# Kernel optimization log

Hardware: AMD Instinct MI355X
Metric: run time of the kernel (lower is better)

## Reference

```python
import jax, jax.numpy as jnp
import numpy as np

D = 2048          # n_embd
F = 1408          # moe_inter_dim
E = 8             # n_routed_experts
TOPK = 2          # n_activated_experts
N_SHARED = 2
ROUTE_SCALE = 1.0


def setup_inputs() -> dict:
    key = jax.random.key(0)
    ks = jax.random.split(key, 8)
    s = 0.02
    x = jax.random.normal(ks[0], (2, 1024, D), dtype=jnp.float32)
    gate_w = jax.random.normal(ks[1], (D, E), dtype=jnp.float32) * s
    Fs = F * N_SHARED
    sw1 = jax.random.normal(ks[2], (D, Fs), dtype=jnp.float32) * s
    sw2 = jax.random.normal(ks[3], (Fs, D), dtype=jnp.float32) * s
    sw3 = jax.random.normal(ks[4], (D, Fs), dtype=jnp.float32) * s
    rw1 = jax.random.normal(ks[5], (E, D, F), dtype=jnp.float32) * s
    rw2 = jax.random.normal(ks[6], (E, F, D), dtype=jnp.float32) * s
    rw3 = jax.random.normal(ks[7], (E, D, F), dtype=jnp.float32) * s
    return {"x": x, "gate_w": gate_w, "sw1": sw1, "sw2": sw2, "sw3": sw3,
            "rw1": rw1, "rw2": rw2, "rw3": rw3}


def _swiglu(x, w1, w2, w3):
    return (jax.nn.silu(x @ w1) * (x @ w3)) @ w2


def reference(x, gate_w, sw1, sw2, sw3, rw1, rw2, rw3):
    B, T, _ = x.shape
    xf = x.reshape(-1, D)                       # [N, D]
    N = xf.shape[0]
    # shared experts (always applied)
    y = _swiglu(xf, sw1, sw2, sw3)              # [N, D]
    # gate: softmax scores, top-k (bias is None since n_embd != 7168; n_groups == 1)
    scores = jax.nn.softmax(xf @ gate_w, axis=-1)       # [N, E]
    weights, indices = jax.lax.top_k(scores, TOPK)       # gathered original scores
    weights = weights * ROUTE_SCALE
    # combine weights per (token, expert); zero for unassigned -> same math as
    # the per-expert gather/scatter loop in the original module
    cw = jnp.zeros((N, E), dtype=xf.dtype).at[jnp.arange(N)[:, None], indices].add(weights)
    for e in range(E):  # fixed small structural loop over experts
        h = _swiglu(xf, rw1[e], rw2[e], rw3[e])  # [N, D]
        y = y + cw[:, e:e + 1] * h
    return y.reshape(B, T, D)
```

## Files before the change

kernel.cpp:

```cpp
#include <hip/hip_runtime.h>
#include <hip/hip_bf16.h>
#include <math.h>

#define D_DIM 2048
#define F_DIM 1408
#define FS_DIM 2816
#define E_NUM 8
#define N_TOK 2048

typedef __attribute__((ext_vector_type(8))) short bf16x8;
typedef __attribute__((ext_vector_type(4))) float f32x4;

#define WAITVM(n) asm volatile("s_waitcnt vmcnt(" #n ")" ::: "memory")

__device__ inline short f2bf(float f) {
    __hip_bfloat16 h = __float2bfloat16(f);
    return *reinterpret_cast<short*>(&h);
}
__device__ inline float bf2f(short s) {
    __hip_bfloat16 h; *reinterpret_cast<short*>(&h) = s;
    return __bfloat162float(h);
}
__device__ inline float silu1(float v) { return v / (1.f + expf(-v)); }

__device__ inline void async_copy16(const void* g, void* l) {
    __builtin_amdgcn_global_load_lds(
        (const __attribute__((address_space(1))) void*)g,
        (__attribute__((address_space(3))) void*)l, 16, 0, 0);
}

__device__ inline void t64h(const float* in, short* out, int K, int N,
                            int kt, int nt, float (*tile)[65], int t)
{
    int k0 = kt * 64, n0 = nt * 64;
    int tr = t >> 4, tc4 = (t & 15) * 4;
#pragma unroll
    for (int i = 0; i < 4; ++i) {
        int r = tr + i * 16;
        float4 v = *reinterpret_cast<const float4*>(in + (size_t)(k0 + r) * N + n0 + tc4);
        tile[r][tc4 + 0] = v.x; tile[r][tc4 + 1] = v.y;
        tile[r][tc4 + 2] = v.z; tile[r][tc4 + 3] = v.w;
    }
    __syncthreads();
#pragma unroll
    for (int i = 0; i < 4; ++i) {
        int n = tr + i * 16;
        short4 s4;
        s4.x = f2bf(tile[tc4 + 0][n]);
        s4.y = f2bf(tile[tc4 + 1][n]);
        s4.z = f2bf(tile[tc4 + 2][n]);
        s4.w = f2bf(tile[tc4 + 3][n]);
        *reinterpret_cast<short4*>(out + (size_t)(n0 + n) * K + k0 + tc4) = s4;
    }
}

__global__ __launch_bounds__(256) void prep_kernel(
    const float* __restrict__ x, const float* __restrict__ gw,
    float* __restrict__ assign_w, int* __restrict__ expert_count,
    int* __restrict__ expert_list, short* __restrict__ Xb,
    const float* __restrict__ sw1, short* __restrict__ swt1,
    const float* __restrict__ sw3, short* __restrict__ swt3,
    const float* __restrict__ rw1, short* __restrict__ rwt1,
    const float* __restrict__ rw3, short* __restrict__ rwt3)
{
    __shared__ float tile[64][65];
    int bid = blockIdx.x;
    int tid = threadIdx.x;
    if (bid < 512) {
        int wid = bid * 4 + (tid >> 6);
        int lane = tid & 63;
        const float* xr = x + (size_t)wid * D_DIM;
        float p[E_NUM];
#pragma unroll
        for (int e = 0; e < E_NUM; ++e) p[e] = 0.f;
        for (int d = lane; d < D_DIM; d += 64) {
            float xv = xr[d];
            const float4* g = reinterpret_cast<const float4*>(gw + (size_t)d * E_NUM);
            float4 g0 = g[0], g1 = g[1];
            p[0] = fmaf(xv, g0.x, p[0]); p[1] = fmaf(xv, g0.y, p[1]);
            p[2] = fmaf(xv, g0.z, p[2]); p[3] = fmaf(xv, g0.w, p[3]);
            p[4] = fmaf(xv, g1.x, p[4]); p[5] = fmaf(xv, g1.y, p[5]);
            p[6] = fmaf(xv, g1.z, p[6]); p[7] = fmaf(xv, g1.w, p[7]);
        }
#pragma unroll
        for (int off = 32; off > 0; off >>= 1)
#pragma unroll
            for (int e = 0; e < E_NUM; ++e)
                p[e] += __shfl_xor(p[e], off, 64);
        if (lane == 0) {
            float m = p[0];
#pragma unroll
            for (int e = 1; e < E_NUM; ++e) m = fmaxf(m, p[e]);
            float s = 0.f, pr[E_NUM];
#pragma unroll
            for (int e = 0; e < E_NUM; ++e) { pr[e] = expf(p[e] - m); s += pr[e]; }
            float inv = 1.f / s;
#pragma unroll
            for (int e = 0; e < E_NUM; ++e) pr[e] *= inv;
            int i0 = 0;
#pragma unroll
            for (int e = 1; e < E_NUM; ++e) if (pr[e] > pr[i0]) i0 = e;
            int i1 = (i0 == 0) ? 1 : 0;
#pragma unroll
            for (int e = 0; e < E_NUM; ++e) if (e != i0 && pr[e] > pr[i1]) i1 = e;
            int s0 = wid * 2, s1 = wid * 2 + 1;
            assign_w[s0] = pr[i0];
            assign_w[s1] = pr[i1];
            int p0 = atomicAdd(&expert_count[i0], 1);
            expert_list[i0 * N_TOK + p0] = s0;
            int p1 = atomicAdd(&expert_count[i1], 1);
            expert_list[i1 * N_TOK + p1] = s1;
        }
    } else if (bid < 2560) {
        int i = ((bid - 512) * 256 + tid) * 8;
        float4 v0 = *reinterpret_cast<const float4*>(x + i);
        float4 v1 = *reinterpret_cast<const float4*>(x + i + 4);
        bf16x8 o;
        o[0] = f2bf(v0.x); o[1] = f2bf(v0.y); o[2] = f2bf(v0.z); o[3] = f2bf(v0.w);
        o[4] = f2bf(v1.x); o[5] = f2bf(v1.y); o[6] = f2bf(v1.z); o[7] = f2bf(v1.w);
        *reinterpret_cast<bf16x8*>(Xb + i) = o;
    } else if (bid < 3968) {
        int t = bid - 2560;
        t64h(sw1, swt1, D_DIM, FS_DIM, t % 32, t / 32, tile, tid);
    } else if (bid < 5376) {
        int t = bid - 3968;
        t64h(sw3, swt3, D_DIM, FS_DIM, t % 32, t / 32, tile, tid);
    } else if (bid < 11008) {
        int t = bid - 5376;
        int e = t / 704, r = t % 704;
        t64h(rw1 + (size_t)e * D_DIM * F_DIM, rwt1 + (size_t)e * F_DIM * D_DIM,
             D_DIM, F_DIM, r % 32, r / 32, tile, tid);
    } else {
        int t = bid - 11008;
        int e = t / 704, r = t % 704;
        t64h(rw3 + (size_t)e * D_DIM * F_DIM, rwt3 + (size_t)e * F_DIM * D_DIM,
             D_DIM, F_DIM, r % 32, r / 32, tile, tid);
    }
}

__global__ __launch_bounds__(512) void moe_in_kernel(
    const short* __restrict__ Xb,
    const short* __restrict__ swt1, const short* __restrict__ swt3, short* __restrict__ Hs,
    const short* __restrict__ rwt1, const short* __restrict__ rwt3, short* __restrict__ Hr,
    const int* __restrict__ expert_list, const int* __restrict__ expert_count,
    const float* __restrict__ sw2, short* __restrict__ swt2,
    const float* __restrict__ rw2, short* __restrict__ rwt2)
{
    __shared__ char SMEM[131072];
    int bid = blockIdx.x, tid = threadIdx.x;

    if (bid >= 896) {
        int t2 = (bid - 896) * 2 + (tid >> 8);
        int t256 = tid & 255;
        float (*tile)[65] = reinterpret_cast<float (*)[65]>(SMEM + (tid >> 8) * 16640);
        if (t2 < 1408) {
            t64h(sw2, swt2, FS_DIM, D_DIM, t2 % 44, t2 / 44, tile, t256);
        } else {
            int r = t2 - 1408;
            int e = r / 704, rr = r % 704;
            t64h(rw2 + (size_t)e * F_DIM * D_DIM, rwt2 + (size_t)e * D_DIM * F_DIM,
                 F_DIM, D_DIM, rr % 22, rr / 22, tile, t256);
        }
        return;
    }

    int xcd = bid & 7, qq = bid >> 3, mtile = qq & 7, gq = qq >> 3;
    int g = gq * 8 + xcd;
    if (g >= 110) return;
    bool gather;
    const short *W1, *W3;
    short* H;
    int ldH, n0, count;
    const int* list = nullptr;
    int m0 = mtile * 256;
    if (g < 22) {
        gather = false; count = N_TOK;
        W1 = swt1; W3 = swt3; H = Hs; ldH = FS_DIM; n0 = g * 128;
    } else {
        int g2 = g - 22, e = g2 / 11;
        n0 = (g2 % 11) * 128;
        gather = true;
        count = expert_count[e];
        if (m0 >= count) return;
        list = expert_list + e * N_TOK;
        W1 = rwt1 + (size_t)e * F_DIM * D_DIM;
        W3 = rwt3 + (size_t)e * F_DIM * D_DIM;
        H = Hr; ldH = F_DIM;
    }

    int l = tid & 63, w = tid >> 6;
    int wm = w >> 2, wn = w & 3, frow = l & 15, fkg = l >> 4;

    const char* aS[2];
#pragma unroll
    for (int j = 0; j < 2; ++j) {
        int u = j * 512 + tid, r = u >> 2, s = u & 3;
        int rr = m0 + r;
        int tok = gather ? ((rr < count) ? (list[rr] >> 1) : 0) : rr;
        aS[j] = (const char*)Xb + (size_t)tok * 4096 + ((s ^ (r & 3)) << 4);
    }
    int brr = tid >> 2, bss = tid & 3;
    size_t boff = (size_t)(n0 + brr) * 4096 + ((bss ^ (brr & 3)) << 4);
    const char* b1S = (const char*)W1 + boff;
    const char* b3S = (const char*)W3 + boff;

    f32x4 acc1[8][2], acc3[8][2];
#pragma unroll
    for (int i = 0; i < 8; ++i)
#pragma unroll
        for (int j = 0; j < 2; ++j) { acc1[i][j] = (f32x4)0.f; acc3[i][j] = (f32x4)0.f; }

#pragma unroll
    for (int p = 0; p < 3; ++p) {
        char* base = SMEM + p * 32768;
        int kb = p << 6;
        async_copy16(aS[0] + kb, base + tid * 16);
        async_copy16(aS[1] + kb, base + (512 + tid) * 16);
        async_copy16(b1S + kb, base + 16384 + tid * 16);
        async_copy16(b3S + kb, base + 24576 + tid * 16);
    }

    for (int t = 0; t < 64; ++t) {
        const char* base = SMEM + (t & 3) * 32768;
        int ts = (t + 3 < 64) ? (t + 3) : 63;
        char* sbase = SMEM + ((t + 3) & 3) * 32768;
        int skb = ts << 6;
        WAITVM(8);
        __builtin_amdgcn_s_barrier();
        bf16x8 af[8], bf[2];
#pragma unroll
        for (int mf = 0; mf < 8; ++mf) {
            int r = wm * 128 + mf * 16 + frow;
            af[mf] = *reinterpret_cast<const bf16x8*>(
                base + r * 64 + ((fkg ^ (r & 3)) << 4));
        }
#pragma unroll
        for (int nf = 0; nf < 2; ++nf) {
            int rb = wn * 32 + nf * 16 + frow;
            bf[nf] = *reinterpret_cast<const bf16x8*>(
                base + 16384 + rb * 64 + ((fkg ^ (rb & 3)) << 4));
        }
        async_copy16(aS[0] + skb, sbase + tid * 16);
        async_copy16(aS[1] + skb, sbase + (512 + tid) * 16);
        __builtin_amdgcn_s_setprio(1);
#pragma unroll
        for (int mf = 0; mf < 8; ++mf)
#pragma unroll
            for (int nf = 0; nf < 2; ++nf)
                acc1[mf][nf] = __builtin_amdgcn_mfma_f32_16x16x32_bf16(
                    af[mf], bf[nf], acc1[mf][nf], 0, 0, 0);
        __builtin_amdgcn_s_setprio(0);
        __builtin_amdgcn_s_barrier();
#pragma unroll
        for (int nf = 0; nf < 2; ++nf) {
            int rb = wn * 32 + nf * 16 + frow;
            bf[nf] = *reinterpret_cast<const bf16x8*>(
                base + 24576 + rb * 64 + ((fkg ^ (rb & 3)) << 4));
        }
        async_copy16(b1S + skb, sbase + 16384 + tid * 16);
        async_copy16(b3S + skb, sbase + 24576 + tid * 16);
        __builtin_amdgcn_s_setprio(1);
#pragma unroll
        for (int mf = 0; mf < 8; ++mf)
#pragma unroll
            for (int nf = 0; nf < 2; ++nf)
                acc3[mf][nf] = __builtin_amdgcn_mfma_f32_16x16x32_bf16(
                    af[mf], bf[nf], acc3[mf][nf], 0, 0, 0);
        __builtin_amdgcn_s_setprio(0);
    }
    WAITVM(0);

#pragma unroll
    for (int mf = 0; mf < 8; ++mf) {
#pragma unroll
        for (int jj = 0; jj < 4; ++jj) {
            int rl = wm * 128 + mf * 16 + fkg * 4 + jj;
            int rr = m0 + rl;
            int s;
            if (gather) { if (rr >= count) continue; s = list[rr]; }
            else s = rr;
            short* hp = H + (size_t)s * ldH + n0 + wn * 32 + frow;
#pragma unroll
            for (int nf = 0; nf < 2; ++nf)
                hp[nf * 16] = f2bf(silu1(acc1[mf][nf][jj]) * acc3[mf][nf][jj]);
        }
    }
}

__global__ __launch_bounds__(512) void moe_out_kernel(
    const short* __restrict__ Hs, const short* __restrict__ swt2, float* __restrict__ Y,
    const short* __restrict__ Hr, const short* __restrict__ rwt2, short* __restrict__ H2,
    const int* __restrict__ expert_list, const int* __restrict__ expert_count)
{
    __shared__ char SMEM[98304];
    int bid = blockIdx.x, tid = threadIdx.x;
    int xcd = bid & 7, qq = bid >> 3, mtile = qq & 7, gq = qq >> 3;
    int g = gq * 8 + xcd;
    if (g >= 144) return;
    bool gather;
    const short *A, *B;
    int ldKb, NIT, n0, count;
    const int* list = nullptr;
    int m0 = mtile * 256;
    if (g < 16) {
        gather = false; count = N_TOK;
        A = Hs; ldKb = FS_DIM * 2; NIT = 88; B = swt2; n0 = g * 128;
    } else {
        int g2 = g - 16, e = g2 >> 4;
        n0 = (g2 & 15) * 128;
        gather = true;
        count = expert_count[e];
        if (m0 >= count) return;
        list = expert_list + e * N_TOK;
        A = Hr; ldKb = F_DIM * 2; NIT = 44;
        B = rwt2 + (size_t)e * D_DIM * F_DIM;
    }

    int l = tid & 63, w = tid >> 6;
    int wm = w >> 2, wn = w & 3, frow = l & 15, fkg = l >> 4;

    const char* aS[2];
#pragma unroll
    for (int j = 0; j < 2; ++j) {
        int u = j * 512 + tid, r = u >> 2, s = u & 3;
        int rr = m0 + r;
        int arow = gather ? ((rr < count) ? list[rr] : 0) : rr;
        aS[j] = (const char*)A + (size_t)arow * ldKb + ((s ^ (r & 3)) << 4);
    }
    int brr = tid >> 2, bss = tid & 3;
    const char* bS = (const char*)B + (size_t)(n0 + brr) * ldKb + ((bss ^ (brr & 3)) << 4);

    f32x4 acc[8][2];
#pragma unroll
    for (int i = 0; i < 8; ++i)
#pragma unroll
        for (int j = 0; j < 2; ++j) acc[i][j] = (f32x4)0.f;

#pragma unroll
    for (int p = 0; p < 3; ++p) {
        char* base = SMEM + p * 24576;
        int kb = p << 6;
        async_copy16(aS[0] + kb, base + tid * 16);
        async_copy16(aS[1] + kb, base + (512 + tid) * 16);
        async_copy16(bS + kb, base + 16384 + tid * 16);
    }

    for (int t = 0; t < NIT; ++t) {
        const char* base = SMEM + (t & 3) * 24576;
        int ts = (t + 3 < NIT) ? (t + 3) : (NIT - 1);
        char* sbase = SMEM + ((t + 3) & 3) * 24576;
        int skb = ts << 6;
        WAITVM(6);
        __builtin_amdgcn_s_barrier();
        bf16x8 af[8], bf0, bf1;
#pragma unroll
        for (int mf = 0; mf < 8; ++mf) {
            int r = wm * 128 + mf * 16 + frow;
            af[mf] = *reinterpret_cast<const bf16x8*>(
                base + r * 64 + ((fkg ^ (r & 3)) << 4));
        }
        {
            int rb = wn * 32 + frow;
            bf0 = *reinterpret_cast<const bf16x8*>(
                base + 16384 + rb * 64 + ((fkg ^ (rb & 3)) << 4));
        }
        async_copy16(aS[0] + skb, sbase + tid * 16);
        async_copy16(aS[1] + skb, sbase + (512 + tid) * 16);
        __builtin_amdgcn_s_setprio(1);
#pragma unroll
        for (int mf = 0; mf < 8; ++mf)
            acc[mf][0] = __builtin_amdgcn_mfma_f32_16x16x32_bf16(
                af[mf], bf0, acc[mf][0], 0, 0, 0);
        __builtin_amdgcn_s_setprio(0);
        __builtin_amdgcn_s_barrier();
        {
            int rb = wn * 32 + 16 + frow;
            bf1 = *reinterpret_cast<const bf16x8*>(
                base + 16384 + rb * 64 + ((fkg ^ (rb & 3)) << 4));
        }
        async_copy16(bS + skb, sbase + 16384 + tid * 16);
        __builtin_amdgcn_s_setprio(1);
#pragma unroll
        for (int mf = 0; mf < 8; ++mf)
            acc[mf][1] = __builtin_amdgcn_mfma_f32_16x16x32_bf16(
                af[mf], bf1, acc[mf][1], 0, 0, 0);
        __builtin_amdgcn_s_setprio(0);
    }
    WAITVM(0);

#pragma unroll
    for (int mf = 0; mf < 8; ++mf) {
#pragma unroll
        for (int jj = 0; jj < 4; ++jj) {
            int rl = wm * 128 + mf * 16 + fkg * 4 + jj;
            int rr = m0 + rl;
            int s;
            if (gather) { if (rr >= count) continue; s = list[rr]; }
            else s = rr;
            int col = n0 + wn * 32 + frow;
            if (!gather) {
                float* op = Y + (size_t)s * D_DIM + col;
                op[0] = acc[mf][0][jj];
                op[16] = acc[mf][1][jj];
            } else {
                short* op = H2 + (size_t)s * D_DIM + col;
                op[0] = f2bf(acc[mf][0][jj]);
                op[16] = f2bf(acc[mf][1][jj]);
            }
        }
    }
}

__global__ __launch_bounds__(256) void combine_kernel(
    float* __restrict__ Y, const short* __restrict__ H2,
    const float* __restrict__ assign_w)
{
    int tok = blockIdx.x, tid = threadIdx.x;
    float w0 = assign_w[2 * tok];
    float w1 = assign_w[2 * tok + 1];
    const short* h0 = H2 + (size_t)(2 * tok) * D_DIM + tid * 8;
    const short* h1 = h0 + D_DIM;
    bf16x8 a = *reinterpret_cast<const bf16x8*>(h0);
    bf16x8 b = *reinterpret_cast<const bf16x8*>(h1);
    float* y = Y + (size_t)tok * D_DIM + tid * 8;
    float4 y0 = *reinterpret_cast<float4*>(y);
    float4 y1 = *reinterpret_cast<float4*>(y + 4);
    y0.x = fmaf(w0, bf2f(a[0]), fmaf(w1, bf2f(b[0]), y0.x));
    y0.y = fmaf(w0, bf2f(a[1]), fmaf(w1, bf2f(b[1]), y0.y));
    y0.z = fmaf(w0, bf2f(a[2]), fmaf(w1, bf2f(b[2]), y0.z));
    y0.w = fmaf(w0, bf2f(a[3]), fmaf(w1, bf2f(b[3]), y0.w));
    y1.x = fmaf(w0, bf2f(a[4]), fmaf(w1, bf2f(b[4]), y1.x));
    y1.y = fmaf(w0, bf2f(a[5]), fmaf(w1, bf2f(b[5]), y1.y));
    y1.z = fmaf(w0, bf2f(a[6]), fmaf(w1, bf2f(b[6]), y1.z));
    y1.w = fmaf(w0, bf2f(a[7]), fmaf(w1, bf2f(b[7]), y1.w));
    *reinterpret_cast<float4*>(y) = y0;
    *reinterpret_cast<float4*>(y + 4) = y1;
}

extern "C" void kernel_launch(void* const* d_in, const int* in_sizes, int n_in,
                              void* d_out, int out_size, void* d_ws, size_t ws_size,
                              hipStream_t stream) {
    const float* x   = (const float*)d_in[0];
    const float* gw  = (const float*)d_in[1];
    const float* sw1 = (const float*)d_in[2];
    const float* sw2 = (const float*)d_in[3];
    const float* sw3 = (const float*)d_in[4];
    const float* rw1 = (const float*)d_in[5];
    const float* rw2 = (const float*)d_in[6];
    const float* rw3 = (const float*)d_in[7];
    float* Y = (float*)d_out;

    char* ws = (char*)d_ws;
    float* assign_w     = (float*)(ws);
    int*   expert_count = (int*)(ws + 16384);
    int*   expert_list  = (int*)(ws + 16384 + 256);

    const size_t XB_OFF   = 131072;
    const size_t SWT1_OFF = XB_OFF + 8388608ull;
    const size_t SWT3_OFF = SWT1_OFF + 11534336ull;
    const size_t SWT2_OFF = SWT3_OFF + 11534336ull;
    const size_t RWT1_OFF = SWT2_OFF + 11534336ull;
    const size_t RWT3_OFF = RWT1_OFF + 46137344ull;
    const size_t RWT2_OFF = RWT3_OFF + 46137344ull;
    const size_t HS_OFF   = RWT2_OFF + 46137344ull;
    const size_t HR_OFF   = HS_OFF + 11534336ull;
    const size_t H2_OFF   = HR_OFF + 11534336ull;

    short* Xb   = (short*)(ws + XB_OFF);
    short* swt1 = (short*)(ws + SWT1_OFF);
    short* swt3 = (short*)(ws + SWT3_OFF);
    short* swt2 = (short*)(ws + SWT2_OFF);
    short* rwt1 = (short*)(ws + RWT1_OFF);
    short* rwt3 = (short*)(ws + RWT3_OFF);
    short* rwt2 = (short*)(ws + RWT2_OFF);
    short* Hs   = (short*)(ws + HS_OFF);
    short* Hr   = (short*)(ws + HR_OFF);
    short* H2   = (short*)(ws + H2_OFF);

    hipMemsetAsync(expert_count, 0, E_NUM * sizeof(int), stream);

    prep_kernel<<<16640, 256, 0, stream>>>(
        x, gw, assign_w, expert_count, expert_list, Xb,
        sw1, swt1, sw3, swt3, rw1, rwt1, rw3, rwt3);

    moe_in_kernel<<<4416, 512, 0, stream>>>(
        Xb, swt1, swt3, Hs, rwt1, rwt3, Hr,
        expert_list, expert_count, sw2, swt2, rw2, rwt2);

    moe_out_kernel<<<1152, 512, 0, stream>>>(
        Hs, swt2, Y, Hr, rwt2, H2, expert_list, expert_count);

    combine_kernel<<<N_TOK, 256, 0, stream>>>(Y, H2, assign_w);
}
```

Baseline: 412.0 us.

## Widen moe_out tile to 256x256 and change LDS swizzle pattern

The down-projection kernel now computes 256-column output tiles instead of 128, doubling the B-tile loaded per stage, halving the grid and giving each wave four accumulator fragments for more A-fragment reuse. The LDS stage grows to 32KB with 128KB total shared memory. The XOR swizzle in both GEMM kernels changes to use row bits 1-2 rather than 0-1, to reduce LDS bank conflicts on fragment reads. The larger tile cuts redundant A loads, but it raises register and LDS pressure and leaves fewer blocks, which risks lower occupancy and poorer load balance across the sparse expert tiles.

```diff
diff --git a/kernel.cpp b/kernel.cpp
--- a/kernel.cpp
+++ b/kernel.cpp
@@ -28,6 +28,8 @@
         (const __attribute__((address_space(1))) void*)g,
         (__attribute__((address_space(3))) void*)l, 16, 0, 0);
 }
+
+#define SWZ(r, s) (((s) ^ (((r) >> 1) & 3)) << 4)
 
 __device__ inline void t64h(const float* in, short* out, int K, int N,
                             int kt, int nt, float (*tile)[65], int t)
@@ -197,10 +199,10 @@
         int u = j * 512 + tid, r = u >> 2, s = u & 3;
         int rr = m0 + r;
         int tok = gather ? ((rr < count) ? (list[rr] >> 1) : 0) : rr;
-        aS[j] = (const char*)Xb + (size_t)tok * 4096 + ((s ^ (r & 3)) << 4);
+        aS[j] = (const char*)Xb + (size_t)tok * 4096 + SWZ(r, s);
     }
     int brr = tid >> 2, bss = tid & 3;
-    size_t boff = (size_t)(n0 + brr) * 4096 + ((bss ^ (brr & 3)) << 4);
+    size_t boff = (size_t)(n0 + brr) * 4096 + SWZ(brr, bss);
     const char* b1S = (const char*)W1 + boff;
     const char* b3S = (const char*)W3 + boff;
 
@@ -231,14 +233,12 @@
 #pragma unroll
         for (int mf = 0; mf < 8; ++mf) {
             int r = wm * 128 + mf * 16 + frow;
-            af[mf] = *reinterpret_cast<const bf16x8*>(
-                base + r * 64 + ((fkg ^ (r & 3)) << 4));
+            af[mf] = *reinterpret_cast<const bf16x8*>(base + r * 64 + SWZ(r, fkg));
         }
 #pragma unroll
         for (int nf = 0; nf < 2; ++nf) {
             int rb = wn * 32 + nf * 16 + frow;
-            bf[nf] = *reinterpret_cast<const bf16x8*>(
-                base + 16384 + rb * 64 + ((fkg ^ (rb & 3)) << 4));
+            bf[nf] = *reinterpret_cast<const bf16x8*>(base + 16384 + rb * 64 + SWZ(rb, fkg));
         }
         async_copy16(aS[0] + skb, sbase + tid * 16);
         async_copy16(aS[1] + skb, sbase + (512 + tid) * 16);
@@ -254,8 +254,7 @@
 #pragma unroll
         for (int nf = 0; nf < 2; ++nf) {
             int rb = wn * 32 + nf * 16 + frow;
-            bf[nf] = *reinterpret_cast<const bf16x8*>(
-                base + 24576 + rb * 64 + ((fkg ^ (rb & 3)) << 4));
+            bf[nf] = *reinterpret_cast<const bf16x8*>(base + 24576 + rb * 64 + SWZ(rb, fkg));
         }
         async_copy16(b1S + skb, sbase + 16384 + tid * 16);
         async_copy16(b3S + skb, sbase + 24576 + tid * 16);
@@ -292,22 +291,22 @@
     const short* __restrict__ Hr, const short* __restrict__ rwt2, short* __restrict__ H2,
     const int* __restrict__ expert_list, const int* __restrict__ expert_count)
 {
-    __shared__ char SMEM[98304];
+    __shared__ char SMEM[131072];
     int bid = blockIdx.x, tid = threadIdx.x;
     int xcd = bid & 7, qq = bid >> 3, mtile = qq & 7, gq = qq >> 3;
     int g = gq * 8 + xcd;
-    if (g >= 144) return;
+    if (g >= 72) return;
     bool gather;
     const short *A, *B;
     int ldKb, NIT, n0, count;
     const int* list = nullptr;
     int m0 = mtile * 256;
-    if (g < 16) {
+    if (g < 8) {
         gather = false; count = N_TOK;
-        A = Hs; ldKb = FS_DIM * 2; NIT = 88; B = swt2; n0 = g * 128;
+        A = Hs; ldKb = FS_DIM * 2; NIT = 88; B = swt2; n0 = g * 256;
     } else {
-        int g2 = g - 16, e = g2 >> 4;
-        n0 = (g2 & 15) * 128;
+        int g2 = g - 8, e = g2 >> 3;
+        n0 = (g2 & 7) * 256;
         gather = true;
         count = expert_count[e];
         if (m0 >= count) return;
@@ -325,65 +324,74 @@
         int u = j * 512 + tid, r = u >> 2, s = u & 3;
         int rr = m0 + r;
         int arow = gather ? ((rr < count) ? list[rr] : 0) : rr;
-        aS[j] = (const char*)A + (size_t)arow * ldKb + ((s ^ (r & 3)) << 4);
-    }
-    int brr = tid >> 2, bss = tid & 3;
-    const char* bS = (const char*)B + (size_t)(n0 + brr) * ldKb + ((bss ^ (brr & 3)) << 4);
-
-    f32x4 acc[8][2];
+        aS[j] = (const char*)A + (size_t)arow * ldKb + SWZ(r, s);
+    }
+    const char* bS[2];
+#pragma unroll
+    for (int j = 0; j < 2; ++j) {
+        int u = j * 512 + tid, r = u >> 2, s = u & 3;
+        bS[j] = (const char*)B + (size_t)(n0 + r) * ldKb + SWZ(r, s);
+    }
+
+    f32x4 acc[8][4];
 #pragma unroll
     for (int i = 0; i < 8; ++i)
 #pragma unroll
-        for (int j = 0; j < 2; ++j) acc[i][j] = (f32x4)0.f;
+        for (int j = 0; j < 4; ++j) acc[i][j] = (f32x4)0.f;
 
 #pragma unroll
     for (int p = 0; p < 3; ++p) {
-        char* base = SMEM + p * 24576;
+        char* base = SMEM + p * 32768;
         int kb = p << 6;
         async_copy16(aS[0] + kb, base + tid * 16);
         async_copy16(aS[1] + kb, base + (512 + tid) * 16);
-        async_copy16(bS + kb, base + 16384 + tid * 16);
+        async_copy16(bS[0] + kb, base + 16384 + tid * 16);
+        async_copy16(bS[1] + kb, base + 16384 + (512 + tid) * 16);
     }
 
     for (int t = 0; t < NIT; ++t) {
-        const char* base = SMEM + (t & 3) * 24576;
+        const char* base = SMEM + (t & 3) * 32768;
         int ts = (t + 3 < NIT) ? (t + 3) : (NIT - 1);
-        char* sbase = SMEM + ((t + 3) & 3) * 24576;
+        char* sbase = SMEM + ((t + 3) & 3) * 32768;
         int skb = ts << 6;
-        WAITVM(6);
+        WAITVM(8);
         __builtin_amdgcn_s_barrier();
-        bf16x8 af[8], bf0, bf1;
+        bf16x8 af[8], bf[4];
 #pragma unroll
         for (int mf = 0; mf < 8; ++mf) {
             int r = wm * 128 + mf * 16 + frow;
-            af[mf] = *reinterpret_cast<const bf16x8*>(
-                base + r * 64 + ((fkg ^ (r & 3)) << 4));
-        }
-        {
-            int rb = wn * 32 + frow;
-            bf0 = *reinterpret_cast<const bf16x8*>(
-                base + 16384 + rb * 64 + ((fkg ^ (rb & 3)) << 4));
+            af[mf] = *reinterpret_cast<const bf16x8*>(base + r * 64 + SWZ(r, fkg));
+        }
+#pragma unroll
+        for (int nf = 0; nf < 2; ++nf) {
+            int rb = wn * 64 + nf * 16 + frow;
+            bf[nf] = *reinterpret_cast<const bf16x8*>(base + 16384 + rb * 64 + SWZ(rb, fkg));
         }
         async_copy16(aS[0] + skb, sbase + tid * 16);
         async_copy16(aS[1] + skb, sbase + (512 + tid) * 16);
         __builtin_amdgcn_s_setprio(1);
 #pragma unroll
         for (int mf = 0; mf < 8; ++mf)
-            acc[mf][0] = __builtin_amdgcn_mfma_f32_16x16x32_bf16(
-                af[mf], bf0, acc[mf][0], 0, 0, 0);
+#pragma unroll
+            for (int nf = 0; nf < 2; ++nf)
+                acc[mf][nf] = __builtin_amdgcn_mfma_f32_16x16x32_bf16(
+                    af[mf], bf[nf], acc[mf][nf], 0, 0, 0);
         __builtin_amdgcn_s_setprio(0);
         __builtin_amdgcn_s_barrier();
-        {
-            int rb = wn * 32 + 16 + frow;
-            bf1 = *reinterpret_cast<const bf16x8*>(
-                base + 16384 + rb * 64 + ((fkg ^ (rb & 3)) << 4));
-        }
-        async_copy16(bS + skb, sbase + 16384 + tid * 16);
+#pragma unroll
+        for (int nf = 2; nf < 4; ++nf) {
+            int rb = wn * 64 + nf * 16 + frow;
+            bf[nf] = *reinterpret_cast<const bf16x8*>(base + 16384 + rb * 64 + SWZ(rb, fkg));
+        }
+        async_copy16(bS[0] + skb, sbase + 16384 + tid * 16);
+        async_copy16(bS[1] + skb, sbase + 16384 + (512 + tid) * 16);
         __builtin_amdgcn_s_setprio(1);
 #pragma unroll
         for (int mf = 0; mf < 8; ++mf)
-            acc[mf][1] = __builtin_amdgcn_mfma_f32_16x16x32_bf16(
-                af[mf], bf1, acc[mf][1], 0, 0, 0);
+#pragma unroll
+            for (int nf = 2; nf < 4; ++nf)
+                acc[mf][nf] = __builtin_amdgcn_mfma_f32_16x16x32_bf16(
+                    af[mf], bf[nf], acc[mf][nf], 0, 0, 0);
         __builtin_amdgcn_s_setprio(0);
     }
     WAITVM(0);
@@ -397,15 +405,17 @@
             int s;
             if (gather) { if (rr >= count) continue; s = list[rr]; }
             else s = rr;
-            int col = n0 + wn * 32 + frow;
+            int col = n0 + wn * 64 + frow;
             if (!gather) {
                 float* op = Y + (size_t)s * D_DIM + col;
-                op[0] = acc[mf][0][jj];
-                op[16] = acc[mf][1][jj];
+#pragma unroll
+                for (int nf = 0; nf < 4; ++nf)
+                    op[nf * 16] = acc[mf][nf][jj];
             } else {
                 short* op = H2 + (size_t)s * D_DIM + col;
-                op[0] = f2bf(acc[mf][0][jj]);
-                op[16] = f2bf(acc[mf][1][jj]);
+#pragma unroll
+                for (int nf = 0; nf < 4; ++nf)
+                    op[nf * 16] = f2bf(acc[mf][nf][jj]);
             }
         }
     }
@@ -487,7 +497,7 @@
         Xb, swt1, swt3, Hs, rwt1, rwt3, Hr,
         expert_list, expert_count, sw2, swt2, rw2, rwt2);
 
-    moe_out_kernel<<<1152, 512, 0, stream>>>(
+    moe_out_kernel<<<576, 512, 0, stream>>>(
         Hs, swt2, Y, Hr, rwt2, H2, expert_list, expert_count);
 
     combine_kernel<<<N_TOK, 256, 0, stream>>>(Y, H2, assign_w);
```

Measured after the change: 381.5 us. 7.4% less time.
